# Kernel tuning notes

Hardware: AMD Instinct MI355X
Metric: run time of the kernel (lower is better)

Reference implementation:

```python
import jax, jax.numpy as jnp
import numpy as np

C = 256          # channels
K = 7            # involution kernel size
GC = 16          # group_channels (fixed in source)
G = C // GC      # groups = 16
RED = C // 4     # reduction channels = 64
B, H, W = 4, 56, 56


def setup_inputs() -> dict:
    key = jax.random.key(0)
    k0, k1, k2 = jax.random.split(key, 3)
    x = jax.random.normal(k0, (B, C, H, W), jnp.float32)
    w1 = jax.random.normal(k1, (RED, C), jnp.float32) * (1.0 / np.sqrt(C))
    b1 = jnp.zeros((RED,), jnp.float32)
    w2 = jax.random.normal(k2, (K * K * G, RED), jnp.float32) * (1.0 / np.sqrt(RED))
    b2 = jnp.zeros((K * K * G,), jnp.float32)
    return {"x": x, "w1": w1, "b1": b1, "w2": w2, "b2": b2}


def reference(x, w1, b1, w2, b2):
    b, c, h, w = x.shape
    # 1x1 conv generator: conv1 (C -> C/4) + ReLU, conv2 (C/4 -> K^2*G)
    t = jax.nn.relu(jnp.einsum('bchw,oc->bohw', x, w1) + b1[None, :, None, None])
    weight = jnp.einsum('bohw,ko->bkhw', t, w2) + b2[None, :, None, None]
    weight = weight.reshape(b, G, K * K, h, w)             # (b, G, K^2, h, w)
    # unfold: patches ordered (C, kh, kw) channel-slowest, matching torch.nn.Unfold
    pad = (K - 1) // 2
    patches = jax.lax.conv_general_dilated_patches(
        x, (K, K), (1, 1), [(pad, pad), (pad, pad)],
        dimension_numbers=('NCHW', 'OIHW', 'NCHW'))        # (b, C*K*K, h, w)
    patches = patches.reshape(b, G, GC, K * K, h, w)
    # per-pixel, per-group weighted sum over the K^2 window positions
    out = jnp.einsum('bgkhw,bgckhw->bgchw', weight, patches)
    return out.reshape(b, c, h, w)
```

## Files before the change

### kernel.cpp

```cpp
#include <hip/hip_runtime.h>

#define B_    4
#define C_    256
#define Kk    7
#define GC_   16
#define G_    16
#define RED_  64
#define H_    56
#define W_    56
#define HW_   3136
#define KK_   49
#define KG_   784
#define NP_   12544

typedef float  f4    __attribute__((ext_vector_type(4)));
typedef float  f32x4 __attribute__((ext_vector_type(4)));
typedef __bf16 bf16x8 __attribute__((ext_vector_type(8)));
typedef __bf16 bf16x4 __attribute__((ext_vector_type(4)));
typedef unsigned short u16;
typedef u16    u16x4 __attribute__((ext_vector_type(4)));
typedef u16    u16x8 __attribute__((ext_vector_type(8)));

__device__ __forceinline__ f4 ld4(const float* p) { return *(const f4*)p; }
__device__ __forceinline__ void st4(float* p, f4 v) { *(f4*)p = v; }
__device__ __forceinline__ float bf2f(u16 u) {
    return __uint_as_float(((unsigned)u) << 16);
}

__global__ __launch_bounds__(256) void xt_kernel(const float* __restrict__ x,
                                                 __bf16* __restrict__ xt) {
    __shared__ __bf16 lt[64][68];
    const int tid = threadIdx.x;
    const int P0  = blockIdx.x * 64;
    const int c0  = blockIdx.y * 64;
    const int b   = P0 / HW_;
    const int p0  = P0 - b * HW_;

    const int pq  = tid & 15;
    const int crb = tid >> 4;
#pragma unroll
    for (int i = 0; i < 4; ++i) {
        const int cr = crb + i * 16;
        const f4 v = ld4(x + (size_t)(b * C_ + c0 + cr) * HW_ + p0 + pq * 4);
#pragma unroll
        for (int j = 0; j < 4; ++j) lt[pq * 4 + j][cr] = (__bf16)v[j];
    }
    __syncthreads();
    const int cq  = tid & 15;
    const int plb = tid >> 4;
#pragma unroll
    for (int i = 0; i < 4; ++i) {
        const int pl = plb + i * 16;
        const bf16x4 rv = *(const bf16x4*)&lt[pl][cq * 4];
        *(bf16x4*)(xt + (size_t)(P0 + pl) * C_ + c0 + cq * 4) = rv;
    }
}

__global__ __launch_bounds__(256) void gen1m2(const __bf16* __restrict__ xt,
                                              const float* __restrict__ w1,
                                              const float* __restrict__ b1,
                                              __bf16* __restrict__ t) {
    __shared__ __bf16 w1s[64][260];
    const int tid  = threadIdx.x;
    const int lane = tid & 63;
    const int wave = tid >> 6;
    const int row  = lane & 15;
    const int kg   = lane >> 4;
    const int P0w  = blockIdx.x * 64 + wave * 16;

    const __bf16* bp = xt + (size_t)(P0w + row) * C_ + kg * 8;
    bf16x8 bv[8];
#pragma unroll
    for (int ks = 0; ks < 8; ++ks) bv[ks] = *(const bf16x8*)(bp + ks * 32);

#pragma unroll
    for (int i = 0; i < 16; ++i) {
        const int q  = tid + i * 256;
        const int r  = q >> 6;
        const int c0 = (q & 63) * 4;
        const f4 v = ld4(w1 + (size_t)r * C_ + c0);
        bf16x4 pk;
#pragma unroll
        for (int j = 0; j < 4; ++j) pk[j] = (__bf16)v[j];
        *(bf16x4*)&w1s[r][c0] = pk;
    }
    __syncthreads();

    f32x4 acc[4] = {f32x4(0.f), f32x4(0.f), f32x4(0.f), f32x4(0.f)};
#pragma unroll
    for (int ks = 0; ks < 8; ++ks)
#pragma unroll
        for (int mt = 0; mt < 4; ++mt) {
            const bf16x8 af = *(const bf16x8*)&w1s[mt * 16 + row][ks * 32 + kg * 8];
            acc[mt] = __builtin_amdgcn_mfma_f32_16x16x32_bf16(af, bv[ks], acc[mt], 0, 0, 0);
        }

#pragma unroll
    for (int mt = 0; mt < 4; ++mt) {
        const f4 bias = ld4(b1 + mt * 16 + kg * 4);
        bf16x4 pk;
#pragma unroll
        for (int j = 0; j < 4; ++j)
            pk[j] = (__bf16)fmaxf(acc[mt][j] + bias[j], 0.f);
        *(bf16x4*)(t + (size_t)(P0w + row) * RED_ + mt * 16 + kg * 4) = pk;
    }
}

__global__ __launch_bounds__(256) void gen2_mfma3(const __bf16* __restrict__ t,
                                                  const float* __restrict__ w2,
                                                  const float* __restrict__ b2,
                                                  __bf16* __restrict__ wgt) {
    __shared__ __bf16 w2s[64][68];
    __shared__ u16    sw[4][16][72];
    const int tid  = threadIdx.x;
    const int lane = tid & 63;
    const int wave = tid >> 6;
    const int row  = lane & 15;
    const int kg   = lane >> 4;
    const int Pw   = blockIdx.x * 256 + wave * 64;
    const int b    = Pw / HW_;
    const int pw   = Pw - b * HW_;
    const int k0   = blockIdx.y * 64;
    const int nMt  = (blockIdx.y == 12) ? 1 : 4;

    bf16x8 bfrag[4][2];
#pragma unroll
    for (int cg = 0; cg < 4; ++cg)
#pragma unroll
        for (int ks = 0; ks < 2; ++ks)
            bfrag[cg][ks] = *(const bf16x8*)(t + (size_t)(Pw + cg * 16 + row) * RED_
                                               + ks * 32 + kg * 8);

#pragma unroll
    for (int i = 0; i < 4; ++i) {
        const int q  = tid + i * 256;
        const int r  = q >> 4;
        const int c0 = (q & 15) * 4;
        f4 v = {0.f, 0.f, 0.f, 0.f};
        if (k0 + r < KG_) v = ld4(w2 + (size_t)(k0 + r) * RED_ + c0);
        bf16x4 pk;
#pragma unroll
        for (int j = 0; j < 4; ++j) pk[j] = (__bf16)v[j];
        *(bf16x4*)&w2s[r][c0] = pk;
    }
    __syncthreads();

    for (int mt = 0; mt < nMt; ++mt) {
        const bf16x8 afr0 = *(const bf16x8*)&w2s[mt * 16 + row][kg * 8];
        const bf16x8 afr1 = *(const bf16x8*)&w2s[mt * 16 + row][32 + kg * 8];
        f32x4 acc[4] = {f32x4(0.f), f32x4(0.f), f32x4(0.f), f32x4(0.f)};
#pragma unroll
        for (int cg = 0; cg < 4; ++cg) {
            acc[cg] = __builtin_amdgcn_mfma_f32_16x16x32_bf16(afr0, bfrag[cg][0], acc[cg], 0, 0, 0);
            acc[cg] = __builtin_amdgcn_mfma_f32_16x16x32_bf16(afr1, bfrag[cg][1], acc[cg], 0, 0, 0);
        }
        const f4 bias = ld4(b2 + k0 + mt * 16 + kg * 4);
#pragma unroll
        for (int cg = 0; cg < 4; ++cg)
#pragma unroll
            for (int j = 0; j < 4; ++j) {
                const __bf16 v = (__bf16)(acc[cg][j] + bias[j]);
                sw[wave][kg * 4 + j][cg * 16 + row] = *(const u16*)&v;
            }
#pragma unroll
        for (int u = 0; u < 2; ++u) {
            const int r16 = (lane >> 3) + u * 8;
            const int ch  = lane & 7;
            const u16x8 v = *(const u16x8*)&sw[wave][r16][ch * 8];
            *(u16x8*)((u16*)wgt + ((size_t)b * KG_ + k0 + mt * 16 + r16) * HW_
                                + pw + ch * 8) = v;
        }
    }
}

#define BR_  4
#define XR_  10
#define XST_ 68
__global__ __launch_bounds__(256) void inv_kernel(const float* __restrict__ x,
                                                  const u16* __restrict__ wgt,
                                                  float* __restrict__ out) {
    __shared__ float xs[GC_][XR_][XST_];
    const int tid = threadIdx.x;
    const int r0  = blockIdx.x * BR_;
    const int g   = blockIdx.y;
    const int b   = blockIdx.z;

    for (int idx = tid; idx < GC_ * XR_ * 16; idx += 256) {
        const int c   = idx / (XR_ * 16);
        const int rem = idx - c * (XR_ * 16);
        const int hr  = rem >> 4;
        const int wq  = rem & 15;
        const int h   = r0 - 3 + hr;
        f4 v = {0.f, 0.f, 0.f, 0.f};
        if (h >= 0 && h < H_) {
            const float* xr_ = x + (size_t)(b * C_ + g * GC_ + c) * HW_ + h * W_;
            const int w0 = wq * 4 - 3;
            if (wq >= 1 && wq <= 13) {
                v = ld4(xr_ + w0);
            } else {
#pragma unroll
                for (int j = 0; j < 4; ++j) {
                    const int w = w0 + j;
                    if (w >= 0 && w < W_) v[j] = xr_[w];
                }
            }
        }
        *(f4*)&xs[c][hr][wq * 4] = v;
    }
    __syncthreads();

    if (tid >= 224) return;
    const int cq  = tid % 14;
    const int r   = (tid / 14) & 3;
    const int cg4 = tid / 56;

    const u16* wb = wgt + ((size_t)b * KG_ + (size_t)g * KK_) * HW_
                        + (r0 + r) * W_ + cq * 4;

    f4 acc[4] = {f4(0.f), f4(0.f), f4(0.f), f4(0.f)};
#pragma unroll
    for (int kh = 0; kh < Kk; ++kh) {
        float tf[7][4];
#pragma unroll
        for (int kw = 0; kw < 7; ++kw) {
            const u16x4 tv = *(const u16x4*)(wb + (size_t)(kh * 7 + kw) * HW_);
#pragma unroll
            for (int j = 0; j < 4; ++j) tf[kw][j] = bf2f(tv[j]);
        }
        const int hr = r + kh;
#pragma unroll
        for (int ci = 0; ci < 4; ++ci) {
            const float* xrow = &xs[cg4 * 4 + ci][hr][cq * 4];
            const f4 x0 = ld4(xrow), x1 = ld4(xrow + 4), x2 = ld4(xrow + 8);
            float xw[12];
#pragma unroll
            for (int j = 0; j < 4; ++j) { xw[j] = x0[j]; xw[4 + j] = x1[j]; xw[8 + j] = x2[j]; }
#pragma unroll
            for (int kw = 0; kw < 7; ++kw)
#pragma unroll
                for (int j = 0; j < 4; ++j)
                    acc[ci][j] = fmaf(tf[kw][j], xw[j + kw], acc[ci][j]);
        }
    }

#pragma unroll
    for (int ci = 0; ci < 4; ++ci)
        st4(out + (size_t)(b * C_ + g * GC_ + cg4 * 4 + ci) * HW_ + (r0 + r) * W_ + cq * 4,
            acc[ci]);
}

extern "C" void kernel_launch(void* const* d_in, const int* in_sizes, int n_in,
                              void* d_out, int out_size, void* d_ws, size_t ws_size,
                              hipStream_t stream) {
    const float* x  = (const float*)d_in[0];
    const float* w1 = (const float*)d_in[1];
    const float* b1 = (const float*)d_in[2];
    const float* w2 = (const float*)d_in[3];
    const float* b2 = (const float*)d_in[4];
    float* out = (float*)d_out;

    char* ws = (char*)d_ws;
    __bf16* xt  = (__bf16*)ws;
    __bf16* t   = (__bf16*)(ws + (size_t)NP_ * C_ * 2);
    __bf16* wgt = (__bf16*)(ws + (size_t)NP_ * C_ * 2 + (size_t)NP_ * RED_ * 2);

    xt_kernel  <<<dim3(NP_ / 64, C_ / 64), 256, 0, stream>>>(x, xt);
    gen1m2     <<<dim3(NP_ / 64),          256, 0, stream>>>(xt, w1, b1, t);
    gen2_mfma3 <<<dim3(NP_ / 256, 13),     256, 0, stream>>>(t, w2, b2, wgt);
    inv_kernel <<<dim3(14, G_, B_),        256, 0, stream>>>(x, (const u16*)wgt, out);
}
```

Baseline: 115.6 us.

## Fuse transpose into gen1 GEMM and split involution channels across blocks

The separate x-transpose kernel is folded into the first generator GEMM: each block loads its 64 pixels × 256 channels of x straight into LDS as bf16, and w1 is staged in two halves to fit LDS. This removes the intermediate xt buffer's global write and read plus one launch. Separately, the involution kernel now splits each group's 16 channels across two blocks (8 each), doubling grid size for better occupancy. The cost is that each block reloads the per-pixel weights twice.

```diff
diff --git a/kernel.cpp b/kernel.cpp
--- a/kernel.cpp
+++ b/kernel.cpp
@@ -27,57 +27,37 @@
     return __uint_as_float(((unsigned)u) << 16);
 }
 
-__global__ __launch_bounds__(256) void xt_kernel(const float* __restrict__ x,
-                                                 __bf16* __restrict__ xt) {
-    __shared__ __bf16 lt[64][68];
-    const int tid = threadIdx.x;
-    const int P0  = blockIdx.x * 64;
-    const int c0  = blockIdx.y * 64;
-    const int b   = P0 / HW_;
-    const int p0  = P0 - b * HW_;
-
-    const int pq  = tid & 15;
-    const int crb = tid >> 4;
-#pragma unroll
-    for (int i = 0; i < 4; ++i) {
-        const int cr = crb + i * 16;
-        const f4 v = ld4(x + (size_t)(b * C_ + c0 + cr) * HW_ + p0 + pq * 4);
-#pragma unroll
-        for (int j = 0; j < 4; ++j) lt[pq * 4 + j][cr] = (__bf16)v[j];
-    }
-    __syncthreads();
-    const int cq  = tid & 15;
-    const int plb = tid >> 4;
-#pragma unroll
-    for (int i = 0; i < 4; ++i) {
-        const int pl = plb + i * 16;
-        const bf16x4 rv = *(const bf16x4*)&lt[pl][cq * 4];
-        *(bf16x4*)(xt + (size_t)(P0 + pl) * C_ + c0 + cq * 4) = rv;
-    }
-}
-
-__global__ __launch_bounds__(256) void gen1m2(const __bf16* __restrict__ xt,
-                                              const float* __restrict__ w1,
-                                              const float* __restrict__ b1,
-                                              __bf16* __restrict__ t) {
-    __shared__ __bf16 w1s[64][260];
+__global__ __launch_bounds__(256) void gen1f(const float* __restrict__ x,
+                                             const float* __restrict__ w1,
+                                             const float* __restrict__ b1,
+                                             __bf16* __restrict__ t) {
+    __shared__ __bf16 lt[64][264];
+    __shared__ __bf16 w1s[64][136];
     const int tid  = threadIdx.x;
     const int lane = tid & 63;
     const int wave = tid >> 6;
     const int row  = lane & 15;
     const int kg   = lane >> 4;
-    const int P0w  = blockIdx.x * 64 + wave * 16;
-
-    const __bf16* bp = xt + (size_t)(P0w + row) * C_ + kg * 8;
-    bf16x8 bv[8];
-#pragma unroll
-    for (int ks = 0; ks < 8; ++ks) bv[ks] = *(const bf16x8*)(bp + ks * 32);
-
-#pragma unroll
-    for (int i = 0; i < 16; ++i) {
+    const int P0   = blockIdx.x * 64;
+    const int b    = P0 / HW_;
+    const int p0   = P0 - b * HW_;
+
+    const int pq  = tid & 15;
+    const int crb = tid >> 4;
+#pragma unroll
+    for (int cc = 0; cc < 4; ++cc)
+#pragma unroll
+        for (int i = 0; i < 4; ++i) {
+            const int c = cc * 64 + crb + i * 16;
+            const f4 v = ld4(x + (size_t)(b * C_ + c) * HW_ + p0 + pq * 4);
+#pragma unroll
+            for (int j = 0; j < 4; ++j) lt[pq * 4 + j][c] = (__bf16)v[j];
+        }
+#pragma unroll
+    for (int i = 0; i < 8; ++i) {
         const int q  = tid + i * 256;
-        const int r  = q >> 6;
-        const int c0 = (q & 63) * 4;
+        const int r  = q >> 5;
+        const int c0 = (q & 31) * 4;
         const f4 v = ld4(w1 + (size_t)r * C_ + c0);
         bf16x4 pk;
 #pragma unroll
@@ -88,12 +68,36 @@
 
     f32x4 acc[4] = {f32x4(0.f), f32x4(0.f), f32x4(0.f), f32x4(0.f)};
 #pragma unroll
-    for (int ks = 0; ks < 8; ++ks)
+    for (int ks = 0; ks < 4; ++ks) {
+        const bf16x8 bv = *(const bf16x8*)&lt[wave * 16 + row][ks * 32 + kg * 8];
 #pragma unroll
         for (int mt = 0; mt < 4; ++mt) {
             const bf16x8 af = *(const bf16x8*)&w1s[mt * 16 + row][ks * 32 + kg * 8];
-            acc[mt] = __builtin_amdgcn_mfma_f32_16x16x32_bf16(af, bv[ks], acc[mt], 0, 0, 0);
-        }
+            acc[mt] = __builtin_amdgcn_mfma_f32_16x16x32_bf16(af, bv, acc[mt], 0, 0, 0);
+        }
+    }
+    __syncthreads();
+#pragma unroll
+    for (int i = 0; i < 8; ++i) {
+        const int q  = tid + i * 256;
+        const int r  = q >> 5;
+        const int c0 = (q & 31) * 4;
+        const f4 v = ld4(w1 + (size_t)r * C_ + 128 + c0);
+        bf16x4 pk;
+#pragma unroll
+        for (int j = 0; j < 4; ++j) pk[j] = (__bf16)v[j];
+        *(bf16x4*)&w1s[r][c0] = pk;
+    }
+    __syncthreads();
+#pragma unroll
+    for (int ks = 4; ks < 8; ++ks) {
+        const bf16x8 bv = *(const bf16x8*)&lt[wave * 16 + row][ks * 32 + kg * 8];
+#pragma unroll
+        for (int mt = 0; mt < 4; ++mt) {
+            const bf16x8 af = *(const bf16x8*)&w1s[mt * 16 + row][(ks - 4) * 32 + kg * 8];
+            acc[mt] = __builtin_amdgcn_mfma_f32_16x16x32_bf16(af, bv, acc[mt], 0, 0, 0);
+        }
+    }
 
 #pragma unroll
     for (int mt = 0; mt < 4; ++mt) {
@@ -102,7 +106,7 @@
 #pragma unroll
         for (int j = 0; j < 4; ++j)
             pk[j] = (__bf16)fmaxf(acc[mt][j] + bias[j], 0.f);
-        *(bf16x4*)(t + (size_t)(P0w + row) * RED_ + mt * 16 + kg * 4) = pk;
+        *(bf16x4*)(t + (size_t)(P0 + wave * 16 + row) * RED_ + mt * 16 + kg * 4) = pk;
     }
 }
 
@@ -179,13 +183,15 @@
 __global__ __launch_bounds__(256) void inv_kernel(const float* __restrict__ x,
                                                   const u16* __restrict__ wgt,
                                                   float* __restrict__ out) {
-    __shared__ float xs[GC_][XR_][XST_];
+    __shared__ float xs[8][XR_][XST_];
     const int tid = threadIdx.x;
     const int r0  = blockIdx.x * BR_;
     const int g   = blockIdx.y;
-    const int b   = blockIdx.z;
-
-    for (int idx = tid; idx < GC_ * XR_ * 16; idx += 256) {
+    const int z   = blockIdx.z;
+    const int b   = z >> 1;
+    const int ch0 = (z & 1) * 8;
+
+    for (int idx = tid; idx < 8 * XR_ * 16; idx += 256) {
         const int c   = idx / (XR_ * 16);
         const int rem = idx - c * (XR_ * 16);
         const int hr  = rem >> 4;
@@ -193,7 +199,7 @@
         const int h   = r0 - 3 + hr;
         f4 v = {0.f, 0.f, 0.f, 0.f};
         if (h >= 0 && h < H_) {
-            const float* xr_ = x + (size_t)(b * C_ + g * GC_ + c) * HW_ + h * W_;
+            const float* xr_ = x + (size_t)(b * C_ + g * GC_ + ch0 + c) * HW_ + h * W_;
             const int w0 = wq * 4 - 3;
             if (wq >= 1 && wq <= 13) {
                 v = ld4(xr_ + w0);
@@ -210,14 +216,14 @@
     __syncthreads();
 
     if (tid >= 224) return;
-    const int cq  = tid % 14;
-    const int r   = (tid / 14) & 3;
-    const int cg4 = tid / 56;
+    const int cq = tid % 14;
+    const int r  = (tid / 14) & 3;
+    const int cg = tid / 56;
 
     const u16* wb = wgt + ((size_t)b * KG_ + (size_t)g * KK_) * HW_
                         + (r0 + r) * W_ + cq * 4;
 
-    f4 acc[4] = {f4(0.f), f4(0.f), f4(0.f), f4(0.f)};
+    f4 acc[2] = {f4(0.f), f4(0.f)};
 #pragma unroll
     for (int kh = 0; kh < Kk; ++kh) {
         float tf[7][4];
@@ -229,8 +235,8 @@
         }
         const int hr = r + kh;
 #pragma unroll
-        for (int ci = 0; ci < 4; ++ci) {
-            const float* xrow = &xs[cg4 * 4 + ci][hr][cq * 4];
+        for (int ci = 0; ci < 2; ++ci) {
+            const float* xrow = &xs[cg * 2 + ci][hr][cq * 4];
             const f4 x0 = ld4(xrow), x1 = ld4(xrow + 4), x2 = ld4(xrow + 8);
             float xw[12];
 #pragma unroll
@@ -244,8 +250,9 @@
     }
 
 #pragma unroll
-    for (int ci = 0; ci < 4; ++ci)
-        st4(out + (size_t)(b * C_ + g * GC_ + cg4 * 4 + ci) * HW_ + (r0 + r) * W_ + cq * 4,
+    for (int ci = 0; ci < 2; ++ci)
+        st4(out + (size_t)(b * C_ + g * GC_ + ch0 + cg * 2 + ci) * HW_
+                + (r0 + r) * W_ + cq * 4,
             acc[ci]);
 }
 
@@ -260,12 +267,10 @@
     float* out = (float*)d_out;
 
     char* ws = (char*)d_ws;
-    __bf16* xt  = (__bf16*)ws;
-    __bf16* t   = (__bf16*)(ws + (size_t)NP_ * C_ * 2);
-    __bf16* wgt = (__bf16*)(ws + (size_t)NP_ * C_ * 2 + (size_t)NP_ * RED_ * 2);
-
-    xt_kernel  <<<dim3(NP_ / 64, C_ / 64), 256, 0, stream>>>(x, xt);
-    gen1m2     <<<dim3(NP_ / 64),          256, 0, stream>>>(xt, w1, b1, t);
+    __bf16* t   = (__bf16*)ws;
+    __bf16* wgt = (__bf16*)(ws + (size_t)NP_ * RED_ * 2);
+
+    gen1f      <<<dim3(NP_ / 64),          256, 0, stream>>>(x, w1, b1, t);
     gen2_mfma3 <<<dim3(NP_ / 256, 13),     256, 0, stream>>>(t, w2, b2, wgt);
-    inv_kernel <<<dim3(14, G_, B_),        256, 0, stream>>>(x, (const u16*)wgt, out);
-}
+    inv_kernel <<<dim3(14, G_, 2 * B_),    256, 0, stream>>>(x, (const u16*)wgt, out);
+}
```

Measured after the change: 111.0 us. 1.04x faster.
